# Kernel optimization log

Hardware: AMD Instinct MI355X
Metric: run time of the kernel (lower is better)

## Reference

```python
import jax, jax.numpy as jnp
import numpy as np

A, V, T = 32, 32, 128          # per-modality hidden dims
PF = 128                       # post_fusion_dim
FUSED = (A + 1) * (V + 1) * (T + 1)  # 140481
B = 256


def setup_inputs() -> dict:
    key = jax.random.key(0)
    ks = jax.random.split(key, 9)
    s1 = 1.0 / np.sqrt(FUSED)
    s2 = 1.0 / np.sqrt(PF)
    return {
        "audio_x": jax.random.normal(ks[0], (B, A), dtype=jnp.float32),
        "video_x": jax.random.normal(ks[1], (B, V), dtype=jnp.float32),
        "text_x": jax.random.normal(ks[2], (B, T), dtype=jnp.float32),
        "W1": jax.random.uniform(ks[3], (FUSED, PF), jnp.float32, -s1, s1),
        "b1": jax.random.uniform(ks[4], (PF,), jnp.float32, -s1, s1),
        "W2": jax.random.uniform(ks[5], (PF, PF), jnp.float32, -s2, s2),
        "b2": jax.random.uniform(ks[6], (PF,), jnp.float32, -s2, s2),
        "W3": jax.random.uniform(ks[7], (PF, 1), jnp.float32, -s2, s2),
        "b3": jax.random.uniform(ks[8], (1,), jnp.float32, -s2, s2),
    }


def reference(audio_x, video_x, text_x, W1, b1, W2, b2, W3, b3):
    b = audio_x.shape[0]
    ones = jnp.ones((b, 1), dtype=audio_x.dtype)
    a = jnp.concatenate([ones, audio_x], axis=1)  # (B, A+1)
    v = jnp.concatenate([ones, video_x], axis=1)  # (B, V+1)
    t = jnp.concatenate([ones, text_x], axis=1)   # (B, T+1)
    # trilinear outer product, flattened: (B, (A+1)*(V+1)*(T+1))
    fusion = jnp.einsum("ba,bv,bt->bavt", a, v, t).reshape(b, -1)
    h1 = jax.nn.relu(fusion @ W1 + b1)
    h2 = jax.nn.relu(h1 @ W2 + b2)
    return h2 @ W3 + b3
```

## Files before the change

kernel.cpp:

```cpp
#include <hip/hip_runtime.h>
#include <hip/hip_bf16.h>
#include <stdint.h>

#define BATCH 256
#define PFD 128
#define T1 129
#define NPAIRS 1089
#define BKSTR 72
#define CHUNK 8

typedef short bf16x8 __attribute__((ext_vector_type(8)));
typedef float f32x4 __attribute__((ext_vector_type(4)));

static __device__ __forceinline__ unsigned bits_of(float f){ union{float f;unsigned u;}x;x.f=f;return x.u; }
static __device__ __forceinline__ float float_of(unsigned u){ union{float f;unsigned u;}x;x.u=u;return x.f; }
static __device__ __forceinline__ unsigned pk_bf16(float a, float b){
  union { __hip_bfloat162 h; unsigned u; } c;
  c.h = __float22bfloat162_rn(make_float2(a, b));
  return c.u;
}

__global__ __launch_bounds__(512, 2) void tfn_k1(
    const float* __restrict__ audio, const float* __restrict__ video,
    const float* __restrict__ text, const float* __restrict__ W1,
    unsigned short* __restrict__ part, int S) {
  __shared__ __align__(16) short b_lds[2][PFD * BKSTR];
  __shared__ __align__(16) float av_lds[BATCH * CHUNK];

  const int tid = threadIdx.x;
  const int bk = blockIdx.x;
  const int npb = NPAIRS / S, rem0 = NPAIRS % S;
  const int p0 = bk * npb + (bk < rem0 ? bk : rem0);
  const int np = npb + (bk < rem0 ? 1 : 0);

  const int wave = tid >> 6, lane = tid & 63;
  const int l15 = lane & 15, quad = lane >> 4;
  const int sn = tid & 127, skg = tid >> 7;

  float treg[2][32];
  float t128r[2];
  #pragma unroll
  for (int mt = 0; mt < 2; ++mt) {
    const int m = wave * 32 + mt * 16 + l15;
    t128r[mt] = text[m * 128 + 127];
    #pragma unroll
    for (int ks = 0; ks < 4; ++ks)
      #pragma unroll
      for (int j = 0; j < 8; ++j) {
        const int it = ks * 32 + quad * 8 + j;
        treg[mt][ks * 8 + j] = (it == 0) ? 1.0f : text[m * 128 + it - 1];
      }
  }

  f32x4 acc[2][8];
  #pragma unroll
  for (int a = 0; a < 2; ++a)
    #pragma unroll
    for (int b = 0; b < 8; ++b) acc[a][b] = f32x4{0.f, 0.f, 0.f, 0.f};

  float pf0[16], pf1[16], rv[8];

  for (int c0 = 0; c0 < np; c0 += CHUNK) {
    const int nc = (np - c0) < CHUNK ? (np - c0) : CHUNK;
    const int pbase = p0 + c0;
    __syncthreads();
    if (tid < BATCH) {
      const int m = tid;
      for (int j = 0; j < nc; ++j) {
        int p = pbase + j;
        int ia = p / 33, iv = p - ia * 33;
        float a = (ia == 0) ? 1.0f : audio[m * 32 + ia - 1];
        float v = (iv == 0) ? 1.0f : video[m * 32 + iv - 1];
        av_lds[m * CHUNK + j] = a * v;
      }
    }
    #pragma unroll
    for (int j = 0; j < 8; ++j) {
      int kk = skg * 8 + j;
      rv[j] = (kk < nc) ? W1[((long)(pbase + kk) * T1 + 128) * PFD + sn] : 0.0f;
    }
    {
      const long rb = (long)pbase * T1;
      #pragma unroll
      for (int g = 0; g < 2; ++g)
        #pragma unroll
        for (int j = 0; j < 8; ++j) {
          pf0[g * 8 + j] = W1[(rb + g * 32 + skg * 8 + j) * PFD + sn];
          pf1[g * 8 + j] = W1[(rb + 64 + g * 32 + skg * 8 + j) * PFD + sn];
        }
    }
    for (int sp = 0; sp < nc; ++sp) {
      float avm[2];
      __syncthreads();
      avm[0] = av_lds[(wave * 32 + l15) * CHUNK + sp];
      avm[1] = av_lds[(wave * 32 + 16 + l15) * CHUNK + sp];
      {
        union { bf16x8 v; unsigned u[4]; } w0, w1;
        #pragma unroll
        for (int d = 0; d < 4; ++d) {
          w0.u[d] = pk_bf16(pf0[2 * d], pf0[2 * d + 1]);
          w1.u[d] = pk_bf16(pf0[8 + 2 * d], pf0[8 + 2 * d + 1]);
        }
        *(bf16x8*)&b_lds[0][sn * BKSTR + skg * 8] = w0.v;
        *(bf16x8*)&b_lds[0][sn * BKSTR + 32 + skg * 8] = w1.v;
      }
      if (sp + 1 < nc) {
        const long rb = (long)(pbase + sp + 1) * T1;
        #pragma unroll
        for (int g = 0; g < 2; ++g)
          #pragma unroll
          for (int j = 0; j < 8; ++j)
            pf0[g * 8 + j] = W1[(rb + g * 32 + skg * 8 + j) * PFD + sn];
      }
      __syncthreads();
      #pragma unroll
      for (int ks = 0; ks < 2; ++ks) {
        bf16x8 A0, A1;
        {
          union { bf16x8 v; unsigned u[4]; } c0u, c1u;
          #pragma unroll
          for (int d = 0; d < 4; ++d) {
            c0u.u[d] = pk_bf16(avm[0] * treg[0][ks * 8 + 2 * d], avm[0] * treg[0][ks * 8 + 2 * d + 1]);
            c1u.u[d] = pk_bf16(avm[1] * treg[1][ks * 8 + 2 * d], avm[1] * treg[1][ks * 8 + 2 * d + 1]);
          }
          A0 = c0u.v; A1 = c1u.v;
        }
        #pragma unroll
        for (int nt = 0; nt < 8; ++nt) {
          bf16x8 bf = *(const bf16x8*)&b_lds[0][(nt * 16 + l15) * BKSTR + ks * 32 + quad * 8];
          acc[0][nt] = __builtin_amdgcn_mfma_f32_16x16x32_bf16(A0, bf, acc[0][nt], 0, 0, 0);
          acc[1][nt] = __builtin_amdgcn_mfma_f32_16x16x32_bf16(A1, bf, acc[1][nt], 0, 0, 0);
        }
      }
      __syncthreads();
      {
        union { bf16x8 v; unsigned u[4]; } w0, w1;
        #pragma unroll
        for (int d = 0; d < 4; ++d) {
          w0.u[d] = pk_bf16(pf1[2 * d], pf1[2 * d + 1]);
          w1.u[d] = pk_bf16(pf1[8 + 2 * d], pf1[8 + 2 * d + 1]);
        }
        *(bf16x8*)&b_lds[1][sn * BKSTR + skg * 8] = w0.v;
        *(bf16x8*)&b_lds[1][sn * BKSTR + 32 + skg * 8] = w1.v;
      }
      if (sp + 1 < nc) {
        const long rb = (long)(pbase + sp + 1) * T1 + 64;
        #pragma unroll
        for (int g = 0; g < 2; ++g)
          #pragma unroll
          for (int j = 0; j < 8; ++j)
            pf1[g * 8 + j] = W1[(rb + g * 32 + skg * 8 + j) * PFD + sn];
      }
      __syncthreads();
      #pragma unroll
      for (int ks2 = 0; ks2 < 2; ++ks2) {
        const int ks = 2 + ks2;
        bf16x8 A0, A1;
        {
          union { bf16x8 v; unsigned u[4]; } c0u, c1u;
          #pragma unroll
          for (int d = 0; d < 4; ++d) {
            c0u.u[d] = pk_bf16(avm[0] * treg[0][ks * 8 + 2 * d], avm[0] * treg[0][ks * 8 + 2 * d + 1]);
            c1u.u[d] = pk_bf16(avm[1] * treg[1][ks * 8 + 2 * d], avm[1] * treg[1][ks * 8 + 2 * d + 1]);
          }
          A0 = c0u.v; A1 = c1u.v;
        }
        #pragma unroll
        for (int nt = 0; nt < 8; ++nt) {
          bf16x8 bf = *(const bf16x8*)&b_lds[1][(nt * 16 + l15) * BKSTR + ks2 * 32 + quad * 8];
          acc[0][nt] = __builtin_amdgcn_mfma_f32_16x16x32_bf16(A0, bf, acc[0][nt], 0, 0, 0);
          acc[1][nt] = __builtin_amdgcn_mfma_f32_16x16x32_bf16(A1, bf, acc[1][nt], 0, 0, 0);
        }
      }
    }
    __syncthreads();
    {
      union { bf16x8 v; unsigned u[4]; } w;
      #pragma unroll
      for (int d = 0; d < 4; ++d) w.u[d] = pk_bf16(rv[2 * d], rv[2 * d + 1]);
      *(bf16x8*)&b_lds[0][sn * BKSTR + skg * 8] = w.v;
    }
    __syncthreads();
    {
      bf16x8 A[2];
      #pragma unroll
      for (int mt = 0; mt < 2; ++mt) {
        const int m = wave * 32 + mt * 16 + l15;
        union { bf16x8 v; unsigned u[4]; } c;
        #pragma unroll
        for (int d = 0; d < 4; ++d) {
          int k0 = quad * 8 + 2 * d, k1 = k0 + 1;
          float f0 = (k0 < nc) ? av_lds[m * CHUNK + k0] * t128r[mt] : 0.0f;
          float f1 = (k1 < nc) ? av_lds[m * CHUNK + k1] * t128r[mt] : 0.0f;
          c.u[d] = pk_bf16(f0, f1);
        }
        A[mt] = c.v;
      }
      #pragma unroll
      for (int nt = 0; nt < 8; ++nt) {
        bf16x8 bf = *(const bf16x8*)&b_lds[0][(nt * 16 + l15) * BKSTR + quad * 8];
        acc[0][nt] = __builtin_amdgcn_mfma_f32_16x16x32_bf16(A[0], bf, acc[0][nt], 0, 0, 0);
        acc[1][nt] = __builtin_amdgcn_mfma_f32_16x16x32_bf16(A[1], bf, acc[1][nt], 0, 0, 0);
      }
    }
  }

  #pragma unroll
  for (int mt = 0; mt < 2; ++mt)
    #pragma unroll
    for (int r = 0; r < 4; ++r) {
      const int m = wave * 32 + mt * 16 + quad * 4 + r;
      union { bf16x8 v; unsigned u[4]; } w;
      #pragma unroll
      for (int d = 0; d < 4; ++d) w.u[d] = pk_bf16(acc[mt][2 * d][r], acc[mt][2 * d + 1][r]);
      *(bf16x8*)&part[((size_t)m * S + bk) * PFD + l15 * 8] = w.v;
    }
}

__global__ __launch_bounds__(256) void tfn_k2(
    const unsigned short* __restrict__ part, const float* __restrict__ b1,
    const float* __restrict__ W2, const float* __restrict__ b2,
    const float* __restrict__ W3, const float* __restrict__ b3,
    float* __restrict__ out, int S) {
  __shared__ float sred[256 * 4];
  __shared__ float h1s[PFD];
  __shared__ float a2s[256];
  __shared__ float red[2];
  const int m = blockIdx.x, tid = threadIdx.x;
  const int g = tid & 31, q = tid >> 5;
  const unsigned short* base = part + (size_t)m * S * PFD;
  float s0 = 0, s1 = 0, s2 = 0, s3 = 0;
  for (int bkk = q; bkk < S; bkk += 8) {
    uint2 v = *(const uint2*)&base[(size_t)bkk * PFD + g * 4];
    s0 += float_of(v.x << 16);
    s1 += float_of(v.x & 0xFFFF0000u);
    s2 += float_of(v.y << 16);
    s3 += float_of(v.y & 0xFFFF0000u);
  }
  sred[tid * 4 + 0] = s0; sred[tid * 4 + 1] = s1;
  sred[tid * 4 + 2] = s2; sred[tid * 4 + 3] = s3;
  __syncthreads();
  if (tid < PFD) {
    const int p = tid;
    float h = 0;
    #pragma unroll
    for (int bl = 0; bl < 8; ++bl) h += sred[(bl * 32 + (p >> 2)) * 4 + (p & 3)];
    const int n = (p & 7) * 16 + (p >> 3);
    h1s[n] = fmaxf(h + b1[n], 0.0f);
  }
  __syncthreads();
  const int n = tid & 127, half = tid >> 7;
  float a2 = 0.0f;
  const int k0 = half * 64;
  #pragma unroll 8
  for (int k = 0; k < 64; ++k) a2 += h1s[k0 + k] * W2[(k0 + k) * PFD + n];
  a2s[tid] = a2;
  __syncthreads();
  if (half == 0) {
    float h2 = fmaxf(a2s[n] + a2s[n + 128] + b2[n], 0.0f);
    float pr = h2 * W3[n];
    #pragma unroll
    for (int off = 32; off > 0; off >>= 1) pr += __shfl_down(pr, off);
    if ((tid & 63) == 0) red[tid >> 6] = pr;
  }
  __syncthreads();
  if (tid == 0) out[m] = red[0] + red[1] + b3[0];
}

extern "C" void kernel_launch(void* const* d_in, const int* in_sizes, int n_in,
                              void* d_out, int out_size, void* d_ws, size_t ws_size,
                              hipStream_t stream) {
  const float* audio = (const float*)d_in[0];
  const float* video = (const float*)d_in[1];
  const float* text  = (const float*)d_in[2];
  const float* W1 = (const float*)d_in[3];
  const float* b1 = (const float*)d_in[4];
  const float* W2 = (const float*)d_in[5];
  const float* b2 = (const float*)d_in[6];
  const float* W3 = (const float*)d_in[7];
  const float* b3 = (const float*)d_in[8];
  unsigned short* part = (unsigned short*)d_ws;

  const size_t slab = (size_t)BATCH * PFD * sizeof(unsigned short);
  int S = (int)(ws_size / slab);
  if (S > 256) S = 256;
  if (S < 1) S = 1;

  tfn_k1<<<S, 512, 0, stream>>>(audio, video, text, W1, part, S);
  tfn_k2<<<BATCH, 256, 0, stream>>>(part, b1, W2, b2, W3, b3, (float*)d_out, S);
}
```

Baseline: 146.1 us.

## Cut register pressure and raise occupancy with single-sync ping-pong W1 tiles

Packs the text operand into bf16 pairs in registers, merges the two prefetch buffers into one, and replaces the two-sync-per-half loop with a single barrier per 64-row tile that alternates between two LDS buffers. It also halves the chunk size, raises launch bounds to 4 blocks per CU, and allows up to 512 blocks (workspace permitting). The goal is more resident waves and fewer barriers to hide W1 streaming latency. Storing text pre-rounded to bf16 adds one extra rounding step, and more blocks mean more partial slabs for the reduction kernel to sum.

After: 176.6 us. 20.9% more time.

```diff
diff --git a/kernel.cpp b/kernel.cpp
--- a/kernel.cpp
+++ b/kernel.cpp
@@ -7,7 +7,8 @@
 #define T1 129
 #define NPAIRS 1089
 #define BKSTR 72
-#define CHUNK 8
+#define CHUNK 4
+#define SMAX 512
 
 typedef short bf16x8 __attribute__((ext_vector_type(8)));
 typedef float f32x4 __attribute__((ext_vector_type(4)));
@@ -20,7 +21,7 @@
   return c.u;
 }
 
-__global__ __launch_bounds__(512, 2) void tfn_k1(
+__global__ __launch_bounds__(512, 4) void tfn_k1(
     const float* __restrict__ audio, const float* __restrict__ video,
     const float* __restrict__ text, const float* __restrict__ W1,
     unsigned short* __restrict__ part, int S) {
@@ -37,7 +38,7 @@
   const int l15 = lane & 15, quad = lane >> 4;
   const int sn = tid & 127, skg = tid >> 7;
 
-  float treg[2][32];
+  unsigned treg[2][4][4];
   float t128r[2];
   #pragma unroll
   for (int mt = 0; mt < 2; ++mt) {
@@ -46,9 +47,11 @@
     #pragma unroll
     for (int ks = 0; ks < 4; ++ks)
       #pragma unroll
-      for (int j = 0; j < 8; ++j) {
-        const int it = ks * 32 + quad * 8 + j;
-        treg[mt][ks * 8 + j] = (it == 0) ? 1.0f : text[m * 128 + it - 1];
+      for (int d = 0; d < 4; ++d) {
+        const int it0 = ks * 32 + quad * 8 + 2 * d;
+        const float f0 = (it0 == 0) ? 1.0f : text[m * 128 + it0 - 1];
+        const float f1 = text[m * 128 + it0];
+        treg[mt][ks][d] = pk_bf16(f0, f1);
       }
   }
 
@@ -58,7 +61,7 @@
     #pragma unroll
     for (int b = 0; b < 8; ++b) acc[a][b] = f32x4{0.f, 0.f, 0.f, 0.f};
 
-  float pf0[16], pf1[16], rv[8];
+  float pf[16];
 
   for (int c0 = 0; c0 < np; c0 += CHUNK) {
     const int nc = (np - c0) < CHUNK ? (np - c0) : CHUNK;
@@ -74,114 +77,76 @@
         av_lds[m * CHUNK + j] = a * v;
       }
     }
-    #pragma unroll
-    for (int j = 0; j < 8; ++j) {
-      int kk = skg * 8 + j;
-      rv[j] = (kk < nc) ? W1[((long)(pbase + kk) * T1 + 128) * PFD + sn] : 0.0f;
-    }
     {
       const long rb = (long)pbase * T1;
       #pragma unroll
       for (int g = 0; g < 2; ++g)
         #pragma unroll
-        for (int j = 0; j < 8; ++j) {
-          pf0[g * 8 + j] = W1[(rb + g * 32 + skg * 8 + j) * PFD + sn];
-          pf1[g * 8 + j] = W1[(rb + 64 + g * 32 + skg * 8 + j) * PFD + sn];
-        }
-    }
-    for (int sp = 0; sp < nc; ++sp) {
-      float avm[2];
-      __syncthreads();
-      avm[0] = av_lds[(wave * 32 + l15) * CHUNK + sp];
-      avm[1] = av_lds[(wave * 32 + 16 + l15) * CHUNK + sp];
+        for (int j = 0; j < 8; ++j)
+          pf[g * 8 + j] = W1[(rb + g * 32 + skg * 8 + j) * PFD + sn];
+    }
+    const int ntiles = nc * 2;
+    for (int s = 0; s < ntiles; ++s) {
+      const int boff = (s & 1) * (PFD * BKSTR);
       {
         union { bf16x8 v; unsigned u[4]; } w0, w1;
         #pragma unroll
         for (int d = 0; d < 4; ++d) {
-          w0.u[d] = pk_bf16(pf0[2 * d], pf0[2 * d + 1]);
-          w1.u[d] = pk_bf16(pf0[8 + 2 * d], pf0[8 + 2 * d + 1]);
-        }
-        *(bf16x8*)&b_lds[0][sn * BKSTR + skg * 8] = w0.v;
-        *(bf16x8*)&b_lds[0][sn * BKSTR + 32 + skg * 8] = w1.v;
-      }
-      if (sp + 1 < nc) {
-        const long rb = (long)(pbase + sp + 1) * T1;
+          w0.u[d] = pk_bf16(pf[2 * d], pf[2 * d + 1]);
+          w1.u[d] = pk_bf16(pf[8 + 2 * d], pf[8 + 2 * d + 1]);
+        }
+        *(bf16x8*)&b_lds[0][boff + sn * BKSTR + skg * 8] = w0.v;
+        *(bf16x8*)&b_lds[0][boff + sn * BKSTR + 32 + skg * 8] = w1.v;
+      }
+      if (s + 1 < ntiles) {
+        const long rb = (long)(pbase + ((s + 1) >> 1)) * T1 + ((s + 1) & 1) * 64;
         #pragma unroll
         for (int g = 0; g < 2; ++g)
           #pragma unroll
           for (int j = 0; j < 8; ++j)
-            pf0[g * 8 + j] = W1[(rb + g * 32 + skg * 8 + j) * PFD + sn];
+            pf[g * 8 + j] = W1[(rb + g * 32 + skg * 8 + j) * PFD + sn];
       }
       __syncthreads();
-      #pragma unroll
-      for (int ks = 0; ks < 2; ++ks) {
+      const int jp = s >> 1;
+      float avm[2];
+      avm[0] = av_lds[(wave * 32 + l15) * CHUNK + jp];
+      avm[1] = av_lds[(wave * 32 + 16 + l15) * CHUNK + jp];
+      #pragma unroll
+      for (int ks2 = 0; ks2 < 2; ++ks2) {
+        const int ks = (s & 1) * 2 + ks2;
         bf16x8 A0, A1;
         {
           union { bf16x8 v; unsigned u[4]; } c0u, c1u;
           #pragma unroll
           for (int d = 0; d < 4; ++d) {
-            c0u.u[d] = pk_bf16(avm[0] * treg[0][ks * 8 + 2 * d], avm[0] * treg[0][ks * 8 + 2 * d + 1]);
-            c1u.u[d] = pk_bf16(avm[1] * treg[1][ks * 8 + 2 * d], avm[1] * treg[1][ks * 8 + 2 * d + 1]);
+            unsigned t0 = treg[0][ks][d], t1 = treg[1][ks][d];
+            c0u.u[d] = pk_bf16(float_of(t0 << 16) * avm[0],
+                               float_of(t0 & 0xFFFF0000u) * avm[0]);
+            c1u.u[d] = pk_bf16(float_of(t1 << 16) * avm[1],
+                               float_of(t1 & 0xFFFF0000u) * avm[1]);
           }
           A0 = c0u.v; A1 = c1u.v;
         }
         #pragma unroll
         for (int nt = 0; nt < 8; ++nt) {
-          bf16x8 bf = *(const bf16x8*)&b_lds[0][(nt * 16 + l15) * BKSTR + ks * 32 + quad * 8];
+          bf16x8 bf = *(const bf16x8*)&b_lds[0][boff + (nt * 16 + l15) * BKSTR + ks2 * 32 + quad * 8];
           acc[0][nt] = __builtin_amdgcn_mfma_f32_16x16x32_bf16(A0, bf, acc[0][nt], 0, 0, 0);
           acc[1][nt] = __builtin_amdgcn_mfma_f32_16x16x32_bf16(A1, bf, acc[1][nt], 0, 0, 0);
         }
       }
+    }
+    {
+      const int boff = (ntiles & 1) * (PFD * BKSTR);
+      #pragma unroll
+      for (int j = 0; j < 8; ++j) {
+        int kk = skg * 8 + j;
+        pf[j] = (kk < nc) ? W1[((long)(pbase + kk) * T1 + 128) * PFD + sn] : 0.0f;
+      }
+      union { bf16x8 v; unsigned u[4]; } w;
+      #pragma unroll
+      for (int d = 0; d < 4; ++d) w.u[d] = pk_bf16(pf[2 * d], pf[2 * d + 1]);
+      *(bf16x8*)&b_lds[0][boff + sn * BKSTR + skg * 8] = w.v;
       __syncthreads();
-      {
-        union { bf16x8 v; unsigned u[4]; } w0, w1;
-        #pragma unroll
-        for (int d = 0; d < 4; ++d) {
-          w0.u[d] = pk_bf16(pf1[2 * d], pf1[2 * d + 1]);
-          w1.u[d] = pk_bf16(pf1[8 + 2 * d], pf1[8 + 2 * d + 1]);
-        }
-        *(bf16x8*)&b_lds[1][sn * BKSTR + skg * 8] = w0.v;
-        *(bf16x8*)&b_lds[1][sn * BKSTR + 32 + skg * 8] = w1.v;
-      }
-      if (sp + 1 < nc) {
-        const long rb = (long)(pbase + sp + 1) * T1 + 64;
-        #pragma unroll
-        for (int g = 0; g < 2; ++g)
-          #pragma unroll
-          for (int j = 0; j < 8; ++j)
-            pf1[g * 8 + j] = W1[(rb + g * 32 + skg * 8 + j) * PFD + sn];
-      }
-      __syncthreads();
-      #pragma unroll
-      for (int ks2 = 0; ks2 < 2; ++ks2) {
-        const int ks = 2 + ks2;
-        bf16x8 A0, A1;
-        {
-          union { bf16x8 v; unsigned u[4]; } c0u, c1u;
-          #pragma unroll
-          for (int d = 0; d < 4; ++d) {
-            c0u.u[d] = pk_bf16(avm[0] * treg[0][ks * 8 + 2 * d], avm[0] * treg[0][ks * 8 + 2 * d + 1]);
-            c1u.u[d] = pk_bf16(avm[1] * treg[1][ks * 8 + 2 * d], avm[1] * treg[1][ks * 8 + 2 * d + 1]);
-          }
-          A0 = c0u.v; A1 = c1u.v;
-        }
-        #pragma unroll
-        for (int nt = 0; nt < 8; ++nt) {
-          bf16x8 bf = *(const bf16x8*)&b_lds[1][(nt * 16 + l15) * BKSTR + ks2 * 32 + quad * 8];
-          acc[0][nt] = __builtin_amdgcn_mfma_f32_16x16x32_bf16(A0, bf, acc[0][nt], 0, 0, 0);
-          acc[1][nt] = __builtin_amdgcn_mfma_f32_16x16x32_bf16(A1, bf, acc[1][nt], 0, 0, 0);
-        }
-      }
-    }
-    __syncthreads();
-    {
-      union { bf16x8 v; unsigned u[4]; } w;
-      #pragma unroll
-      for (int d = 0; d < 4; ++d) w.u[d] = pk_bf16(rv[2 * d], rv[2 * d + 1]);
-      *(bf16x8*)&b_lds[0][sn * BKSTR + skg * 8] = w.v;
-    }
-    __syncthreads();
-    {
       bf16x8 A[2];
       #pragma unroll
       for (int mt = 0; mt < 2; ++mt) {
@@ -198,7 +163,7 @@
       }
       #pragma unroll
       for (int nt = 0; nt < 8; ++nt) {
-        bf16x8 bf = *(const bf16x8*)&b_lds[0][(nt * 16 + l15) * BKSTR + quad * 8];
+        bf16x8 bf = *(const bf16x8*)&b_lds[0][boff + (nt * 16 + l15) * BKSTR + quad * 8];
         acc[0][nt] = __builtin_amdgcn_mfma_f32_16x16x32_bf16(A[0], bf, acc[0][nt], 0, 0, 0);
         acc[1][nt] = __builtin_amdgcn_mfma_f32_16x16x32_bf16(A[1], bf, acc[1][nt], 0, 0, 0);
       }
@@ -283,7 +248,7 @@
 
   const size_t slab = (size_t)BATCH * PFD * sizeof(unsigned short);
   int S = (int)(ws_size / slab);
-  if (S > 256) S = 256;
+  if (S > SMAX) S = SMAX;
   if (S < 1) S = 1;
 
   tfn_k1<<<S, 512, 0, stream>>>(audio, video, text, W1, part, S);
```
